# Performance work log

Measured on AMD Instinct MI355X. Metric: run time of the kernel, lower is better.

The kernel has to match this reference:

```python
import jax, jax.numpy as jnp
import numpy as np

B, N, H, D, T = 2, 512, 128, 128, 8  # batch, nodes, feat width, mid/out size, triplet fts
Z = 2 * H  # concat(node_fts, hidden)


def _lin_params(key, fan_in, fan_out):
    kw, kb = jax.random.split(key)
    scale = 1.0 / np.sqrt(fan_in)
    w = jax.random.uniform(kw, (fan_in, fan_out), jnp.float32, -scale, scale)
    b = jax.random.uniform(kb, (fan_out,), jnp.float32, -scale, scale)
    return w, b


def setup_inputs() -> dict:
    key = jax.random.key(0)
    ks = jax.random.split(key, 16)
    inp = {
        'node_fts': jax.random.normal(ks[0], (B, N, H), jnp.float32),
        'edge_fts': jax.random.normal(ks[1], (B, N, N, H), jnp.float32),
        'graph_fts': jax.random.normal(ks[2], (B, H), jnp.float32),
        'adj_mat': (jax.random.uniform(ks[3], (B, N, N)) < 0.5).astype(jnp.float32),
        'hidden': jax.random.normal(ks[4], (B, N, H), jnp.float32),
    }
    # message linears
    inp['Wm1'], inp['bm1'] = _lin_params(ks[5], Z, D)
    inp['Wm2'], inp['bm2'] = _lin_params(ks[6], Z, D)
    inp['Wme'], inp['bme'] = _lin_params(ks[7], H, D)
    inp['Wmg'], inp['bmg'] = _lin_params(ks[8], H, D)
    # output linears
    inp['Wo1'], inp['bo1'] = _lin_params(ks[9], Z, D)
    inp['Wo2'], inp['bo2'] = _lin_params(ks[10], D, D)
    # triplet linears
    inp['Wt1'], inp['bt1'] = _lin_params(ks[11], Z, T)
    inp['Wt2'], inp['bt2'] = _lin_params(ks[12], Z, T)
    inp['Wte'], inp['bte'] = _lin_params(ks[13], H, T)
    inp['Wtg'], inp['btg'] = _lin_params(ks[14], H, T)
    return inp


def reference(node_fts, edge_fts, graph_fts, adj_mat, hidden,
              Wm1, bm1, Wm2, bm2, Wme, bme, Wmg, bmg,
              Wo1, bo1, Wo2, bo2,
              Wt1, bt1, Wt2, bt2, Wte, bte, Wtg, btg):
    z = jnp.concatenate([node_fts, hidden], axis=-1)  # [b,n,2h]

    msg_1 = z @ Wm1 + bm1            # [b,n,d]
    msg_2 = z @ Wm2 + bm2            # [b,n,d]
    msg_e = edge_fts @ Wme + bme     # [b,n,n,d]
    msg_g = graph_fts @ Wmg + bmg    # [b,d]

    # triplet messages: broadcast pairwise sum -> relu, shape [b,n,n,t]
    tri = (z @ Wt1 + bt1)[:, None, :, :] \
        + (z @ Wt2 + bt2)[:, :, None, :] \
        + (edge_fts @ Wte + bte) \
        + (graph_fts @ Wtg + btg)[:, None, None, :]
    tri_msgs = jax.nn.relu(tri)

    # pairwise message broadcast-add, mask by adjacency, max over senders (axis 1)
    msgs = msg_1[:, None, :, :] + msg_2[:, :, None, :] + msg_e \
         + msg_g[:, None, None, :]                      # [b,n,n,d]
    msgs = jnp.max(msgs * adj_mat[..., None], axis=1)   # [b,n,d]

    ret = (z @ Wo1 + bo1) + (msgs @ Wo2 + bo2)           # [b,n,d]
    return (ret, tri_msgs)
```

## Files before the change

### kernel.cpp

```cpp
#include <hip/hip_runtime.h>
#include <hip/hip_bf16.h>

#define NB 2
#define NN 512
#define HH 128
#define DD 128
#define TT 8

#define WPACK_OFF 0
#define C_OFF     36864
#define BROW_OFF  561152
#define TC_OFF    1085440
#define TB_OFF    1118208
#define OC_OFF    1150976
#define PART_OFF  1675264
#define ZF_OFF    18452480

#define OUT_TRI   131072

typedef float f32x4 __attribute__((ext_vector_type(4)));
typedef short s16x8 __attribute__((ext_vector_type(8)));

__device__ __forceinline__ unsigned short f2bf(float f) {
    union { float f; unsigned int u; } x; x.f = f;
    unsigned int u = x.u;
    unsigned int r = (u + 0x7FFFu + ((u >> 16) & 1u)) >> 16;
    return (unsigned short)r;
}

__device__ __forceinline__ unsigned cvt2bf(float a, float b) {
#if __has_builtin(__builtin_amdgcn_cvt_pk_bf16_f32)
    auto r = __builtin_amdgcn_cvt_pk_bf16_f32(a, b);
    return __builtin_bit_cast(unsigned, r);
#else
    return (unsigned)f2bf(a) | ((unsigned)f2bf(b) << 16);
#endif
}

__global__ __launch_bounds__(256) void k0_precompute(
    const float* __restrict__ node, const float* __restrict__ hidden,
    const float* __restrict__ graph,
    const float* __restrict__ Wm1, const float* __restrict__ Wm2,
    const float* __restrict__ Wo1, const float* __restrict__ Wmg,
    const float* __restrict__ Wt1, const float* __restrict__ Wt2,
    const float* __restrict__ Wtg,
    const float* __restrict__ Wme, const float* __restrict__ Wte,
    const float* __restrict__ bm1, const float* __restrict__ bm2,
    const float* __restrict__ bme, const float* __restrict__ bmg,
    const float* __restrict__ bo1, const float* __restrict__ bo2,
    const float* __restrict__ bt1, const float* __restrict__ bt2,
    const float* __restrict__ bte, const float* __restrict__ btg,
    char* __restrict__ ws)
{
    const int bx = blockIdx.x, tid = threadIdx.x;
    if (bx == 256) {
        unsigned short* wp = (unsigned short*)(ws + WPACK_OFF);
        for (int idx = tid; idx < 16 * 144 * 8; idx += 256) {
            int j = idx & 7, tmp = idx >> 3;
            int n = tmp % 144, kq = tmp / 144;
            int k = kq * 8 + j;
            float v = 0.f;
            if (n < 128) v = Wme[k * 128 + n];
            else if (n < 136) v = Wte[k * 8 + (n - 128)];
            wp[idx] = f2bf(v);
        }
        return;
    }
    __shared__ float zs[4 * 257];
    const int row0 = bx * 4;
    const int b = row0 >> 9;
    #pragma unroll
    for (int e = 0; e < 4; e++) {
        int idx = e * 256 + tid;
        int rl = idx >> 8, col = idx & 255;
        float v = (col < 128) ? node[(row0 + rl) * 128 + col]
                              : hidden[(row0 + rl) * 128 + col - 128];
        zs[rl * 257 + col] = v;
    }
    __syncthreads();

    float* Cws = (float*)(ws + C_OFF);
    float* Bws = (float*)(ws + BROW_OFF);
    float* Ows = (float*)(ws + OC_OFF);
    float* TCw = (float*)(ws + TC_OFF);
    float* TBw = (float*)(ws + TB_OFF);

    const int d = tid & 127, half = tid >> 7;
    const float* z0 = zs + (half * 2) * 257;
    const float* z1 = zs + (half * 2 + 1) * 257;
    float c0 = 0.f, c1 = 0.f, q0 = 0.f, q1 = 0.f, o0 = 0.f, o1 = 0.f;
    for (int k = 0; k < 256; k++) {
        float w1 = Wm1[k * 128 + d], w2 = Wm2[k * 128 + d], wo = Wo1[k * 128 + d];
        float za = z0[k], zb = z1[k];
        c0 += za * w1; c1 += zb * w1;
        q0 += za * w2; q1 += zb * w2;
        o0 += za * wo; o1 += zb * wo;
    }
    float gm = 0.f;
    for (int k = 0; k < 128; k++) gm += graph[b * 128 + k] * Wmg[k * 128 + d];
    const float cb = gm + bm1[d] + bm2[d] + bme[d] + bmg[d];
    const float ob = bo1[d] + bo2[d];
    const int r0 = row0 + half * 2;
    Cws[r0 * 128 + d] = c0 + cb;  Cws[(r0 + 1) * 128 + d] = c1 + cb;
    Bws[r0 * 128 + d] = q0;       Bws[(r0 + 1) * 128 + d] = q1;
    Ows[r0 * 128 + d] = o0 + ob;  Ows[(r0 + 1) * 128 + d] = o1 + ob;

    if (tid < 64) {
        int r4 = tid >> 4, t = (tid >> 1) & 7, which = tid & 1;
        const float* zr = zs + r4 * 257;
        const float* W = which ? Wt2 : Wt1;
        float acc = 0.f;
        for (int k = 0; k < 256; k++) acc += zr[k] * W[k * 8 + t];
        int rg = row0 + r4;
        if (which == 0) {
            float gt = 0.f;
            for (int k = 0; k < 128; k++) gt += graph[b * 128 + k] * Wtg[k * 8 + t];
            TCw[rg * 8 + t] = acc + gt + bt1[t] + bt2[t] + bte[t] + btg[t];
        } else {
            TBw[rg * 8 + t] = acc;
        }
    }
}

__global__ __launch_bounds__(512, 2) void k2_main(
    const float* __restrict__ edge, const float* __restrict__ adj,
    char* __restrict__ ws, float* __restrict__ out)
{
    __shared__ float red[8][16][64];
    __shared__ int zflag[16];
    const int tid = threadIdx.x;
    const int jt = blockIdx.x, ic = blockIdx.y, b = blockIdx.z;
    const int j0 = jt * 16, i0 = ic * 64;

    const int lane = tid & 63, wave = tid >> 6;
    const int g = wave >> 2, sq = wave & 3;
    const int quad = lane >> 4, l15 = lane & 15;
    const int ntbase = g * 4;

    if (tid < 16) zflag[tid] = 0;
    __syncthreads();

    const float* Bws = (const float*)(ws + BROW_OFF);
    const float* TCw = (const float*)(ws + TC_OFF);
    const float* TBw = (const float*)(ws + TB_OFF);
    const s16x8* wp8 = (const s16x8*)(ws + WPACK_OFF);
    float* part = (float*)(ws + PART_OFF);
    int* Zws = (int*)(ws + ZF_OFF);

    s16x8 Bf[5][4];
    #pragma unroll
    for (int s = 0; s < 4; s++) {
        #pragma unroll
        for (int ntl = 0; ntl < 5; ntl++) {
            int nt = (ntl < 4) ? (ntbase + ntl) : 8;
            Bf[ntl][s] = wp8[(4 * s + quad) * 144 + nt * 16 + l15];
        }
    }

    const int jb = j0 + quad * 4;
    float TCf[4];
    #pragma unroll
    for (int r = 0; r < 4; r++)
        TCf[r] = (l15 < 8) ? TCw[(b * 512 + jb + r) * 8 + l15] : 0.f;

    float Mx[4][4];
    #pragma unroll
    for (int ntl = 0; ntl < 4; ntl++)
        #pragma unroll
        for (int r = 0; r < 4; r++) Mx[ntl][r] = -INFINITY;
    int anyz[4] = {0, 0, 0, 0};

    const int ig0 = i0 + sq * 16;
    const float* erow = edge + ((b * 512 + ig0) * 512 + j0 + l15) * 128 + quad * 8;

    float4 raw[8];
    #pragma unroll
    for (int s = 0; s < 4; s++) {
        raw[2 * s]     = *(const float4*)(erow + s * 32);
        raw[2 * s + 1] = *(const float4*)(erow + s * 32 + 4);
    }

    for (int ii = 0; ii < 16; ii++) {
        const int ig = ig0 + ii;
        s16x8 af[4];
        #pragma unroll
        for (int s = 0; s < 4; s++) {
            union { s16x8 v; unsigned u[4]; } pk;
            float4 p = raw[2 * s], q = raw[2 * s + 1];
            pk.u[0] = cvt2bf(p.x, p.y);
            pk.u[1] = cvt2bf(p.z, p.w);
            pk.u[2] = cvt2bf(q.x, q.y);
            pk.u[3] = cvt2bf(q.z, q.w);
            af[s] = pk.v;
        }
        if (ii < 15) {
            const float* ernx = erow + (ii + 1) * 65536;
            #pragma unroll
            for (int s = 0; s < 4; s++) {
                raw[2 * s]     = *(const float4*)(ernx + s * 32);
                raw[2 * s + 1] = *(const float4*)(ernx + s * 32 + 4);
            }
        }
        float adjv[4];
        const int arow = (b * 512 + ig) * 512 + jb;
        #pragma unroll
        for (int r = 0; r < 4; r++) adjv[r] = adj[arow + r];
        float brw[4];
        const int br0 = (b * 512 + ig) * 128;
        #pragma unroll
        for (int ntl = 0; ntl < 4; ntl++)
            brw[ntl] = Bws[br0 + (ntbase + ntl) * 16 + l15];
        const float tb = (l15 < 8) ? TBw[(b * 512 + ig) * 8 + l15] : 0.f;

        f32x4 acc[5];
        #pragma unroll
        for (int ntl = 0; ntl < 5; ntl++) acc[ntl] = (f32x4){0.f, 0.f, 0.f, 0.f};
        #pragma unroll
        for (int s = 0; s < 4; s++) {
            #pragma unroll
            for (int ntl = 0; ntl < 5; ntl++)
                acc[ntl] = __builtin_amdgcn_mfma_f32_16x16x32_bf16(
                    af[s], Bf[ntl][s], acc[ntl], 0, 0, 0);
        }
        #pragma unroll
        for (int r = 0; r < 4; r++) {
            const int isz = (adjv[r] == 0.f);
            anyz[r] |= isz;
            #pragma unroll
            for (int ntl = 0; ntl < 4; ntl++) {
                float v = isz ? -INFINITY : (acc[ntl][r] + brw[ntl]);
                Mx[ntl][r] = fmaxf(Mx[ntl][r], v);
            }
        }
        if (g == 1 && l15 < 8) {
            float* tout = out + OUT_TRI + ((b * 512 + ig) * 512 + jb) * 8 + l15;
            #pragma unroll
            for (int r = 0; r < 4; r++) {
                float tv = acc[4][r] + TCf[r] + tb;
                tout[r * 8] = fmaxf(tv, 0.f);
            }
        }
    }

    if (g == 0 && l15 == 0) {
        #pragma unroll
        for (int r = 0; r < 4; r++)
            if (anyz[r]) atomicOr(&zflag[quad * 4 + r], 1);
    }
    #pragma unroll
    for (int ntl = 0; ntl < 4; ntl++)
        #pragma unroll
        for (int r = 0; r < 4; r++)
            red[wave][quad * 4 + r][ntl * 16 + l15] = Mx[ntl][r];
    __syncthreads();

    {
        const int q = tid;
        const int j = q >> 5, dq = q & 31;
        const int g2 = dq >> 4, c0 = (dq & 15) * 4;
        const float* r0p = &red[g2 * 4][j][c0];
        float4 m = *(const float4*)r0p;
        #pragma unroll
        for (int w = 1; w < 4; w++) {
            const float4 o = *(const float4*)&red[g2 * 4 + w][j][c0];
            m.x = fmaxf(m.x, o.x); m.y = fmaxf(m.y, o.y);
            m.z = fmaxf(m.z, o.z); m.w = fmaxf(m.w, o.w);
        }
        *(float4*)(part + ((b * 8 + ic) * 512 + j0 + j) * 128 + dq * 4) = m;
    }
    if (tid < 16) Zws[(b * 8 + ic) * 512 + j0 + tid] = zflag[tid];
}

__global__ __launch_bounds__(128) void k3_final(
    const char* __restrict__ ws, const float* __restrict__ Wo2,
    float* __restrict__ out)
{
    __shared__ float ms[128];
    const int bj = blockIdx.x, d = threadIdx.x;
    const int b = bj >> 9, j = bj & 511;
    const float* part = (const float*)(ws + PART_OFF);
    const int* Zws = (const int*)(ws + ZF_OFF);
    const float* Cws = (const float*)(ws + C_OFF);
    const float* Ows = (const float*)(ws + OC_OFF);

    const int rj = b * 512 + j;
    float m = -INFINITY;
    int zf = 0;
    #pragma unroll
    for (int ic = 0; ic < 8; ic++) {
        m = fmaxf(m, part[((b * 8 + ic) * 512 + j) * 128 + d]);
        zf |= Zws[(b * 8 + ic) * 512 + j];
    }
    float c = Cws[rj * 128 + d];
    float mm = fmaxf(m + c, zf ? 0.f : -INFINITY);
    ms[d] = mm;
    __syncthreads();
    float acc = Ows[rj * 128 + d];
    #pragma unroll 8
    for (int k = 0; k < 128; k++) acc += ms[k] * Wo2[k * 128 + d];
    out[rj * 128 + d] = acc;
}

extern "C" void kernel_launch(void* const* d_in, const int* in_sizes, int n_in,
                              void* d_out, int out_size, void* d_ws, size_t ws_size,
                              hipStream_t stream) {
    const float* node   = (const float*)d_in[0];
    const float* edge   = (const float*)d_in[1];
    const float* graph  = (const float*)d_in[2];
    const float* adj    = (const float*)d_in[3];
    const float* hidden = (const float*)d_in[4];
    const float* Wm1 = (const float*)d_in[5];  const float* bm1 = (const float*)d_in[6];
    const float* Wm2 = (const float*)d_in[7];  const float* bm2 = (const float*)d_in[8];
    const float* Wme = (const float*)d_in[9];  const float* bme = (const float*)d_in[10];
    const float* Wmg = (const float*)d_in[11]; const float* bmg = (const float*)d_in[12];
    const float* Wo1 = (const float*)d_in[13]; const float* bo1 = (const float*)d_in[14];
    const float* Wo2 = (const float*)d_in[15]; const float* bo2 = (const float*)d_in[16];
    const float* Wt1 = (const float*)d_in[17]; const float* bt1 = (const float*)d_in[18];
    const float* Wt2 = (const float*)d_in[19]; const float* bt2 = (const float*)d_in[20];
    const float* Wte = (const float*)d_in[21]; const float* bte = (const float*)d_in[22];
    const float* Wtg = (const float*)d_in[23]; const float* btg = (const float*)d_in[24];
    float* out = (float*)d_out;
    char* ws = (char*)d_ws;

    k0_precompute<<<dim3(257), dim3(256), 0, stream>>>(
        node, hidden, graph, Wm1, Wm2, Wo1, Wmg, Wt1, Wt2, Wtg, Wme, Wte,
        bm1, bm2, bme, bmg, bo1, bo2, bt1, bt2, bte, btg, ws);
    k2_main<<<dim3(32, 8, 2), dim3(512), 0, stream>>>(edge, adj, ws, out);
    k3_final<<<dim3(1024), dim3(128), 0, stream>>>(ws, Wo2, out);
}
```

Measured before the change: 504.8 us.

## Double-buffer edge, adj and bias loads in main loop; split precompute finer

Measured after the change: 500.7 us. Within noise of the previous version (-0.8%).

```diff
diff --git a/kernel.cpp b/kernel.cpp
--- a/kernel.cpp
+++ b/kernel.cpp
@@ -53,7 +53,7 @@
     char* __restrict__ ws)
 {
     const int bx = blockIdx.x, tid = threadIdx.x;
-    if (bx == 256) {
+    if (bx == 512) {
         unsigned short* wp = (unsigned short*)(ws + WPACK_OFF);
         for (int idx = tid; idx < 16 * 144 * 8; idx += 256) {
             int j = idx & 7, tmp = idx >> 3;
@@ -66,16 +66,16 @@
         }
         return;
     }
-    __shared__ float zs[4 * 257];
-    const int row0 = bx * 4;
+    __shared__ float zs[2 * 260];
+    const int row0 = bx * 2;
     const int b = row0 >> 9;
     #pragma unroll
-    for (int e = 0; e < 4; e++) {
+    for (int e = 0; e < 2; e++) {
         int idx = e * 256 + tid;
         int rl = idx >> 8, col = idx & 255;
         float v = (col < 128) ? node[(row0 + rl) * 128 + col]
                               : hidden[(row0 + rl) * 128 + col - 128];
-        zs[rl * 257 + col] = v;
+        zs[rl * 260 + col] = v;
     }
     __syncthreads();
 
@@ -86,35 +86,36 @@
     float* TBw = (float*)(ws + TB_OFF);
 
     const int d = tid & 127, half = tid >> 7;
-    const float* z0 = zs + (half * 2) * 257;
-    const float* z1 = zs + (half * 2 + 1) * 257;
-    float c0 = 0.f, c1 = 0.f, q0 = 0.f, q1 = 0.f, o0 = 0.f, o1 = 0.f;
+    const int row = row0 + half;
+    const float* z = zs + half * 260;
+    float c = 0.f, q = 0.f, o = 0.f;
+    #pragma unroll 8
     for (int k = 0; k < 256; k++) {
-        float w1 = Wm1[k * 128 + d], w2 = Wm2[k * 128 + d], wo = Wo1[k * 128 + d];
-        float za = z0[k], zb = z1[k];
-        c0 += za * w1; c1 += zb * w1;
-        q0 += za * w2; q1 += zb * w2;
-        o0 += za * wo; o1 += zb * wo;
+        float za = z[k];
+        c = fmaf(za, Wm1[k * 128 + d], c);
+        q = fmaf(za, Wm2[k * 128 + d], q);
+        o = fmaf(za, Wo1[k * 128 + d], o);
     }
     float gm = 0.f;
-    for (int k = 0; k < 128; k++) gm += graph[b * 128 + k] * Wmg[k * 128 + d];
+    #pragma unroll 8
+    for (int k = 0; k < 128; k++) gm = fmaf(graph[b * 128 + k], Wmg[k * 128 + d], gm);
     const float cb = gm + bm1[d] + bm2[d] + bme[d] + bmg[d];
-    const float ob = bo1[d] + bo2[d];
-    const int r0 = row0 + half * 2;
-    Cws[r0 * 128 + d] = c0 + cb;  Cws[(r0 + 1) * 128 + d] = c1 + cb;
-    Bws[r0 * 128 + d] = q0;       Bws[(r0 + 1) * 128 + d] = q1;
-    Ows[r0 * 128 + d] = o0 + ob;  Ows[(r0 + 1) * 128 + d] = o1 + ob;
-
-    if (tid < 64) {
-        int r4 = tid >> 4, t = (tid >> 1) & 7, which = tid & 1;
-        const float* zr = zs + r4 * 257;
+    Cws[row * 128 + d] = c + cb;
+    Bws[row * 128 + d] = q;
+    Ows[row * 128 + d] = o + bo1[d] + bo2[d];
+
+    if (tid < 32) {
+        int rl = tid >> 4, t = (tid >> 1) & 7, which = tid & 1;
+        const float* zr = zs + rl * 260;
         const float* W = which ? Wt2 : Wt1;
         float acc = 0.f;
-        for (int k = 0; k < 256; k++) acc += zr[k] * W[k * 8 + t];
-        int rg = row0 + r4;
+        #pragma unroll 8
+        for (int k = 0; k < 256; k++) acc = fmaf(zr[k], W[k * 8 + t], acc);
+        int rg = row0 + rl;
         if (which == 0) {
             float gt = 0.f;
-            for (int k = 0; k < 128; k++) gt += graph[b * 128 + k] * Wtg[k * 8 + t];
+            #pragma unroll 8
+            for (int k = 0; k < 128; k++) gt = fmaf(graph[b * 128 + k], Wtg[k * 8 + t], gt);
             TCw[rg * 8 + t] = acc + gt + bt1[t] + bt2[t] + bte[t] + btg[t];
         } else {
             TBw[rg * 8 + t] = acc;
@@ -173,44 +174,57 @@
     const int ig0 = i0 + sq * 16;
     const float* erow = edge + ((b * 512 + ig0) * 512 + j0 + l15) * 128 + quad * 8;
 
-    float4 raw[8];
-    #pragma unroll
-    for (int s = 0; s < 4; s++) {
-        raw[2 * s]     = *(const float4*)(erow + s * 32);
-        raw[2 * s + 1] = *(const float4*)(erow + s * 32 + 4);
-    }
-
+    float4 raw[2][8];
+    float4 adjn[2];
+    float brwn[2][4];
+    float tbn[2];
+
+    {
+        #pragma unroll
+        for (int s = 0; s < 4; s++) {
+            raw[0][2 * s]     = *(const float4*)(erow + s * 32);
+            raw[0][2 * s + 1] = *(const float4*)(erow + s * 32 + 4);
+        }
+        adjn[0] = *(const float4*)(adj + (b * 512 + ig0) * 512 + jb);
+        const int br0 = (b * 512 + ig0) * 128;
+        #pragma unroll
+        for (int ntl = 0; ntl < 4; ntl++)
+            brwn[0][ntl] = Bws[br0 + (ntbase + ntl) * 16 + l15];
+        tbn[0] = (l15 < 8) ? TBw[(b * 512 + ig0) * 8 + l15] : 0.f;
+    }
+
+    #pragma unroll 2
     for (int ii = 0; ii < 16; ii++) {
+        const int p = ii & 1, pn = p ^ 1;
         const int ig = ig0 + ii;
+
         s16x8 af[4];
         #pragma unroll
         for (int s = 0; s < 4; s++) {
             union { s16x8 v; unsigned u[4]; } pk;
-            float4 p = raw[2 * s], q = raw[2 * s + 1];
-            pk.u[0] = cvt2bf(p.x, p.y);
-            pk.u[1] = cvt2bf(p.z, p.w);
-            pk.u[2] = cvt2bf(q.x, q.y);
-            pk.u[3] = cvt2bf(q.z, q.w);
+            float4 pv = raw[p][2 * s], qv = raw[p][2 * s + 1];
+            pk.u[0] = cvt2bf(pv.x, pv.y);
+            pk.u[1] = cvt2bf(pv.z, pv.w);
+            pk.u[2] = cvt2bf(qv.x, qv.y);
+            pk.u[3] = cvt2bf(qv.z, qv.w);
             af[s] = pk.v;
         }
+
         if (ii < 15) {
             const float* ernx = erow + (ii + 1) * 65536;
             #pragma unroll
             for (int s = 0; s < 4; s++) {
-                raw[2 * s]     = *(const float4*)(ernx + s * 32);
-                raw[2 * s + 1] = *(const float4*)(ernx + s * 32 + 4);
+                raw[pn][2 * s]     = *(const float4*)(ernx + s * 32);
+                raw[pn][2 * s + 1] = *(const float4*)(ernx + s * 32 + 4);
             }
-        }
-        float adjv[4];
-        const int arow = (b * 512 + ig) * 512 + jb;
-        #pragma unroll
-        for (int r = 0; r < 4; r++) adjv[r] = adj[arow + r];
-        float brw[4];
-        const int br0 = (b * 512 + ig) * 128;
-        #pragma unroll
-        for (int ntl = 0; ntl < 4; ntl++)
-            brw[ntl] = Bws[br0 + (ntbase + ntl) * 16 + l15];
-        const float tb = (l15 < 8) ? TBw[(b * 512 + ig) * 8 + l15] : 0.f;
+            const int ign = ig + 1;
+            adjn[pn] = *(const float4*)(adj + (b * 512 + ign) * 512 + jb);
+            const int brn = (b * 512 + ign) * 128;
+            #pragma unroll
+            for (int ntl = 0; ntl < 4; ntl++)
+                brwn[pn][ntl] = Bws[brn + (ntbase + ntl) * 16 + l15];
+            tbn[pn] = (l15 < 8) ? TBw[(b * 512 + ign) * 8 + l15] : 0.f;
+        }
 
         f32x4 acc[5];
         #pragma unroll
@@ -222,13 +236,15 @@
                 acc[ntl] = __builtin_amdgcn_mfma_f32_16x16x32_bf16(
                     af[s], Bf[ntl][s], acc[ntl], 0, 0, 0);
         }
+
+        const float av[4] = {adjn[p].x, adjn[p].y, adjn[p].z, adjn[p].w};
         #pragma unroll
         for (int r = 0; r < 4; r++) {
-            const int isz = (adjv[r] == 0.f);
+            const int isz = (av[r] == 0.f);
             anyz[r] |= isz;
             #pragma unroll
             for (int ntl = 0; ntl < 4; ntl++) {
-                float v = isz ? -INFINITY : (acc[ntl][r] + brw[ntl]);
+                float v = isz ? -INFINITY : (acc[ntl][r] + brwn[p][ntl]);
                 Mx[ntl][r] = fmaxf(Mx[ntl][r], v);
             }
         }
@@ -236,7 +252,7 @@
             float* tout = out + OUT_TRI + ((b * 512 + ig) * 512 + jb) * 8 + l15;
             #pragma unroll
             for (int r = 0; r < 4; r++) {
-                float tv = acc[4][r] + TCf[r] + tb;
+                float tv = acc[4][r] + TCf[r] + tbn[p];
                 tout[r * 8] = fmaxf(tv, 0.f);
             }
         }
@@ -297,7 +313,7 @@
     __syncthreads();
     float acc = Ows[rj * 128 + d];
     #pragma unroll 8
-    for (int k = 0; k < 128; k++) acc += ms[k] * Wo2[k * 128 + d];
+    for (int k = 0; k < 128; k++) acc = fmaf(ms[k], Wo2[k * 128 + d], acc);
     out[rj * 128 + d] = acc;
 }
 
@@ -322,7 +338,7 @@
     float* out = (float*)d_out;
     char* ws = (char*)d_ws;
 
-    k0_precompute<<<dim3(257), dim3(256), 0, stream>>>(
+    k0_precompute<<<dim3(513), dim3(256), 0, stream>>>(
         node, hidden, graph, Wm1, Wm2, Wo1, Wmg, Wt1, Wt2, Wtg, Wme, Wte,
         bm1, bm2, bme, bmg, bo1, bo2, bt1, bt2, bte, btg, ws);
     k2_main<<<dim3(32, 8, 2), dim3(512), 0, stream>>>(edge, adj, ws, out);
```
